# Optimization experiments

Measured on AMD Instinct MI355X. Metric: run time of the kernel, lower is better.

The kernel has to match this reference:

```python
import jax, jax.numpy as jnp
import numpy as np

BIG = 1e30  # stand-in for +inf at DP boundaries (never selected by min)


def setup_inputs() -> dict:
    key = jax.random.key(0)
    kx, kp = jax.random.split(key)
    B, D, T = 32, 16, 1024        # batch, channels (d_patts), stream length
    P, L = 64, 32                 # n_patts, l_patts
    x = jax.random.normal(kx, (B, D, T), dtype=jnp.float32)
    patts = jax.random.normal(kp, (P, D, L), dtype=jnp.float32)
    rho = 0.5
    w = float(rho ** (1.0 / L))   # self.w = rho ** (1 / l_patts)
    return {"x": x, "patts": patts, "w": w}


def _dtw(x, patts, w):
    # Weighted streaming DTW: for each pattern p and each ending time j,
    # D[i, j] = cost[i, j] + min(D[i-1, j], w*D[i, j-1], w*D[i-1, j-1])
    # with D[i, 0] = cost[i, 0] + D[i-1, 0] (first time column cumsum) and
    # cost[i, j] = ||x[:, j] - patts[:, i]||^2 (squared euclidean over channels).
    B, D, T = x.shape
    P, _, L = patts.shape
    p2 = jnp.sum(patts * patts, axis=1)                       # (P, L)

    def cost_at(xj):                                          # xj: (B, D)
        x2 = jnp.sum(xj * xj, axis=1)                         # (B,)
        xp = jnp.einsum('bd,pdl->bpl', xj, patts)             # (B, P, L)
        return x2[:, None, None] + p2[None] - 2.0 * xp        # (B, P, L)

    # first time column
    col0 = jnp.cumsum(cost_at(x[:, :, 0]), axis=-1)           # (B, P, L)

    def step(prev, xj):
        cost = cost_at(xj)                                    # (B, P, L)
        prev_up = jnp.concatenate(
            [jnp.full_like(prev[..., :1], BIG), prev[..., :-1]], axis=-1)
        m = w * jnp.minimum(prev, prev_up)                    # (B, P, L)

        def inner(new_im1, cm):                               # scan along pattern axis
            c_i, m_i = cm
            new_i = c_i + jnp.minimum(new_im1, m_i)
            return new_i, new_i

        _, new = jax.lax.scan(
            inner, jnp.full((B, P), BIG, cost.dtype),
            (jnp.moveaxis(cost, -1, 0), jnp.moveaxis(m, -1, 0)))
        new_col = jnp.moveaxis(new, 0, -1)                    # (B, P, L)
        return new_col, new_col[..., -1]                      # emit full-pattern match cost

    xs = jnp.moveaxis(x[:, :, 1:], -1, 0)                     # (T-1, B, D)
    _, rest = jax.lax.scan(step, col0, xs)                    # (T-1, B, P)
    dtw = jnp.concatenate([col0[None, ..., -1], rest], axis=0)  # (T, B, P)
    return jnp.moveaxis(dtw, 0, -1)                           # (B, P, T)


def reference(x, patts, w):
    return jnp.sqrt(_dtw(x, patts, w))
```

## Files before the change

kernel.cpp:

```cpp
#include <hip/hip_runtime.h>
#include <math.h>

#define B_ 32
#define D_ 16
#define T_ 1024
#define P_ 64
#define L_ 32
#define KB 524288.0f

typedef short short8 __attribute__((ext_vector_type(8)));
typedef float f32x4 __attribute__((ext_vector_type(4)));
typedef unsigned short ushort_t;

template<int CTRL, int ROW_MASK, bool BC>
__device__ __forceinline__ float dpp_mov(float old_, float src) {
  int o = __builtin_bit_cast(int, old_);
  int s = __builtin_bit_cast(int, src);
  int r = __builtin_amdgcn_update_dpp(o, s, CTRL, ROW_MASK, 0xf, BC);
  return __builtin_bit_cast(float, r);
}

__device__ __forceinline__ float scan_sum32(float v) {
  v += dpp_mov<0x111, 0xf, true>(0.f, v);
  v += dpp_mov<0x112, 0xf, true>(0.f, v);
  v += dpp_mov<0x114, 0xf, true>(0.f, v);
  v += dpp_mov<0x118, 0xf, true>(0.f, v);
  v += dpp_mov<0x142, 0xa, false>(0.f, v);
  return v;
}

__device__ __forceinline__ float scan_max32(float v) {
  asm("s_nop 1\n\t"
      "v_max_f32_dpp %0, %0, %0 row_shr:1 row_mask:0xf bank_mask:0xf\n\t"
      "s_nop 1\n\t"
      "v_max_f32_dpp %0, %0, %0 row_shr:2 row_mask:0xf bank_mask:0xf\n\t"
      "s_nop 1\n\t"
      "v_max_f32_dpp %0, %0, %0 row_shr:4 row_mask:0xf bank_mask:0xf\n\t"
      "s_nop 1\n\t"
      "v_max_f32_dpp %0, %0, %0 row_shr:8 row_mask:0xf bank_mask:0xf\n\t"
      "s_nop 1\n\t"
      "v_max_f32_dpp %0, %0, %0 row_bcast:15 row_mask:0xa bank_mask:0xf"
      : "+v"(v));
  return v;
}

__device__ __forceinline__ ushort_t f2bf(float f) {
  unsigned u = __builtin_bit_cast(unsigned, f);
  return (ushort_t)((u + 0x7FFFu + ((u >> 16) & 1u)) >> 16);
}
__device__ __forceinline__ float bf2f(ushort_t h) {
  unsigned u = ((unsigned)h) << 16;
  return __builtin_bit_cast(float, u);
}

__global__ void prep_x(const float* __restrict__ x, ushort_t* __restrict__ xA) {
  int gid = blockIdx.x * blockDim.x + threadIdx.x;
  if (gid >= B_ * T_) return;
  int b = gid >> 10, t = gid & 1023;
  float x2 = 0.f;
  ushort_t o[32];
#pragma unroll
  for (int d = 0; d < 16; ++d) {
    float v = x[((b * 16 + d) << 10) + t];
    x2 = fmaf(v, v, x2);
    o[d] = f2bf(v);
  }
  o[16] = 0x3F80; o[17] = 0x3F80;
  ushort_t hi = f2bf(x2);
  o[18] = hi;
  o[19] = f2bf(x2 - bf2f(hi));
#pragma unroll
  for (int d = 20; d < 32; ++d) o[d] = 0;
  uint4* dst = (uint4*)(xA + (size_t)gid * 32);
#pragma unroll
  for (int q = 0; q < 4; ++q) {
    const ushort_t* s = o + q * 8;
    uint4 u;
    u.x = (unsigned)s[0] | ((unsigned)s[1] << 16);
    u.y = (unsigned)s[2] | ((unsigned)s[3] << 16);
    u.z = (unsigned)s[4] | ((unsigned)s[5] << 16);
    u.w = (unsigned)s[6] | ((unsigned)s[7] << 16);
    dst[q] = u;
  }
}

__global__ __launch_bounds__(64) void prep_patt(const float* __restrict__ patts,
                                                ushort_t* __restrict__ pB) {
  __shared__ float Ls[16 * 33];
  __shared__ float Lh[64];
  __shared__ float LP2[32];

  const int p = blockIdx.x;
  const int l = threadIdx.x;
  const int half = l >> 5;
  const int m = l & 31;

  float p2acc = 0.f;
#pragma unroll
  for (int dd = 0; dd < 16; dd += 2) {
    int d = dd + half;
    float v = patts[((p * 16 + d) << 5) + m];
    p2acc = fmaf(v, v, p2acc);
    Ls[d * 33 + m] = scan_sum32(v);
  }
  Lh[l] = p2acc;
  __syncthreads();
  {
    float tot = Lh[m] + Lh[32 + m];
    float pref = scan_sum32(tot);
    if (half == 0) LP2[m] = pref;
  }
  __syncthreads();

  const int n = l & 15, q = l >> 4;
#pragma unroll
  for (int iblk = 0; iblk < 2; ++iblk) {
    const int i = iblk * 16 + n;
    ushort_t o[8];
    if (q < 2) {
#pragma unroll
      for (int e = 0; e < 8; ++e)
        o[e] = f2bf(-2.f * Ls[(q * 8 + e) * 33 + i]);
    } else if (q == 2) {
      float P2 = LP2[i];
      ushort_t hi = f2bf(P2);
      o[0] = hi; o[1] = f2bf(P2 - bf2f(hi));
      o[2] = f2bf((float)(i + 1)); o[3] = o[2];
      o[4] = o[5] = o[6] = o[7] = 0;
    } else {
#pragma unroll
      for (int e = 0; e < 8; ++e) o[e] = 0;
    }
    uint4 u;
    u.x = (unsigned)o[0] | ((unsigned)o[1] << 16);
    u.y = (unsigned)o[2] | ((unsigned)o[3] << 16);
    u.z = (unsigned)o[4] | ((unsigned)o[5] << 16);
    u.w = (unsigned)o[6] | ((unsigned)o[7] << 16);
    ((uint4*)pB)[(p * 2 + iblk) * 64 + l] = u;
  }
}

__global__ __launch_bounds__(256, 3) void dtw_kernel(
    const ushort_t* __restrict__ xA,
    const ushort_t* __restrict__ pBg,
    const float* __restrict__ wp,
    float* __restrict__ out)
{
  __shared__ float lds[4 * 2640];

  const int tid = threadIdx.x;
  const int l   = tid & 63;
  const int wid = tid >> 6;
  const int li  = l & 31;
  const int g   = l >> 5;
  const int q4  = l >> 4;
  const unsigned bx = blockIdx.x;
  const int ch   = bx % 3u;
  const int rest = bx / 3u;
  const int b     = rest >> 3;
  const int pbase = (rest & 7) << 3;
  const int pA  = pbase + (wid << 1);
  const float w = wp[0];
  const float nw = -w;
  const bool l0c = (li == 0), l31 = (li == 31);

  const int t0    = ch << 4;
  const int warmT = ch ? 16 : 0;

  const short8* pBs = (const short8*)pBg;
  short8 B00 = pBs[((pA    ) * 2 + 0) * 64 + l];
  short8 B01 = pBs[((pA    ) * 2 + 1) * 64 + l];
  short8 B10 = pBs[((pA + 1) * 2 + 0) * 64 + l];
  short8 B11 = pBs[((pA + 1) * 2 + 1) * 64 + l];

  const short8* xAs = (const short8*)xA + ((size_t)b << 12);

  short8 Aa;
  auto loadA = [&](int t) {
    Aa = xAs[((((t0 + t) << 4) + (l & 15)) << 2) + q4];
  };

  float* ldsW = lds + wid * 2640 + 20 + (l & 15) * 20 + q4 * 4;
  const float* ldsR  = lds + wid * 2640 + 20 + g * 660 + li * 20;
  const float* ldsRx = ldsR - 20;

  {
    float* pb = lds + wid * 2640;
    if (l < 20) {
      pb[l] = 0.f; pb[660 + l] = 0.f; pb[1320 + l] = 0.f; pb[1980 + l] = 0.f;
    }
  }
  __syncthreads();

  auto fill = [&](int bufsel) {
    f32x4 z = {0.f, 0.f, 0.f, 0.f};
    float* wb = ldsW + bufsel * 1320;
    f32x4 d0 = __builtin_amdgcn_mfma_f32_16x16x32_bf16(Aa, B00, z, 0, 0, 0);
    f32x4 d1 = __builtin_amdgcn_mfma_f32_16x16x32_bf16(Aa, B01, z, 0, 0, 0);
    f32x4 d2 = __builtin_amdgcn_mfma_f32_16x16x32_bf16(Aa, B10, z, 0, 0, 0);
    f32x4 d3 = __builtin_amdgcn_mfma_f32_16x16x32_bf16(Aa, B11, z, 0, 0, 0);
    *(f32x4*)(wb + 0)   = d0;
    *(f32x4*)(wb + 320) = d1;
    *(f32x4*)(wb + 660) = d2;
    *(f32x4*)(wb + 980) = d3;
  };

  float* orow = out + (((size_t)(b * P_ + pA + g)) << 10) + (t0 << 4);
  float dcur = 0.f;

  auto DP = [&](int bufsel, bool first, bool store, float* op) {
    const float* rb = ldsR  + bufsel * 1320;
    const float* rx = ldsRx + bufsel * 1320;
    f32x4 s0 = *(const f32x4*)(rb + 0);
    f32x4 x0 = *(const f32x4*)(rx + 0);
    f32x4 s1 = *(const f32x4*)(rb + 4);
    f32x4 x1 = *(const f32x4*)(rx + 4);
    f32x4 s2 = *(const f32x4*)(rb + 8);
    f32x4 x2 = *(const f32x4*)(rx + 8);
    f32x4 s3 = *(const f32x4*)(rb + 12);
    f32x4 x3 = *(const f32x4*)(rx + 12);
    float4 r0, r1, r2, r3;
#pragma unroll
    for (int k4 = 0; k4 < 4; ++k4) {
      f32x4 Sq = (k4 == 0) ? s0 : (k4 == 1) ? s1 : (k4 == 2) ? s2 : s3;
      f32x4 Xq = (k4 == 0) ? x0 : (k4 == 1) ? x1 : (k4 == 2) ? x2 : x3;
      float4 rv;
#pragma unroll
      for (int e = 0; e < 4; ++e) {
        float t1  = KB + Xq[e];
        float spk = KB + Sq[e];
        float pu = dpp_mov<0x138, 0xf, true>(0.f, dcur);
        pu = l0c ? dcur : pu;
        float mn = fminf(dcur, pu);
        float u  = fmaf(nw, mn, t1);
        float Mx = scan_max32(u);
        float val = spk - Mx;
        if (first && k4 == 0 && e == 0)
          val = Sq[0];
        dcur = val;
        if (e == 0) rv.x = val; else if (e == 1) rv.y = val;
        else if (e == 2) rv.z = val; else rv.w = val;
      }
      if (k4 == 0) r0 = rv; else if (k4 == 1) r1 = rv;
      else if (k4 == 2) r2 = rv; else r3 = rv;
    }
    if (store) {
      if (l31) {
        float4 s;
        s.x = __builtin_amdgcn_sqrtf(r0.x); s.y = __builtin_amdgcn_sqrtf(r0.y);
        s.z = __builtin_amdgcn_sqrtf(r0.z); s.w = __builtin_amdgcn_sqrtf(r0.w);
        *(float4*)(op + 0) = s;
        s.x = __builtin_amdgcn_sqrtf(r1.x); s.y = __builtin_amdgcn_sqrtf(r1.y);
        s.z = __builtin_amdgcn_sqrtf(r1.z); s.w = __builtin_amdgcn_sqrtf(r1.w);
        *(float4*)(op + 4) = s;
        s.x = __builtin_amdgcn_sqrtf(r2.x); s.y = __builtin_amdgcn_sqrtf(r2.y);
        s.z = __builtin_amdgcn_sqrtf(r2.z); s.w = __builtin_amdgcn_sqrtf(r2.w);
        *(float4*)(op + 8) = s;
        s.x = __builtin_amdgcn_sqrtf(r3.x); s.y = __builtin_amdgcn_sqrtf(r3.y);
        s.z = __builtin_amdgcn_sqrtf(r3.z); s.w = __builtin_amdgcn_sqrtf(r3.w);
        *(float4*)(op + 12) = s;
      }
    }
  };

  loadA(0);
  fill(0);
  loadA(1);
  for (int t = 0; t < 32; ++t) {
    if (t + 1 < 32) fill((t & 1) ^ 1);
    if (t + 2 < 32) loadA(t + 2);
    DP(t & 1, t == 0, t >= warmT, orow + (t << 4));
  }
}

extern "C" void kernel_launch(void* const* d_in, const int* in_sizes, int n_in,
                              void* d_out, int out_size, void* d_ws, size_t ws_size,
                              hipStream_t stream) {
  const float* x     = (const float*)d_in[0];
  const float* patts = (const float*)d_in[1];
  const float* w     = (const float*)d_in[2];
  float* out = (float*)d_out;

  ushort_t* xA = (ushort_t*)d_ws;
  ushort_t* pB = (ushort_t*)((char*)d_ws + (size_t)B_ * T_ * 32 * 2);

  prep_x<<<(B_ * T_ + 255) / 256, 256, 0, stream>>>(x, xA);
  prep_patt<<<P_, 64, 0, stream>>>(patts, pB);
  dtw_kernel<<<B_ * (P_ / 8) * 3, 256, 0, stream>>>(xA, pB, w, out);
}
```

Before: 113.4 us.

## Fuse prep kernels, use single-wave DTW blocks with four uneven time chunks

The two preprocessing kernels become one launch: blocks below 128 pack x and the rest pack four patterns each. The DTW kernel moves from 256-thread blocks covering four pattern pairs to 64-thread single-wave blocks. Time is now split into four overlapping chunks with uneven starts and lengths instead of three equal ones, which gives more and smaller blocks for better CU fill and less per-block latency. The DP inner step is also reformulated: the KB offset is folded into the MFMA accumulator, and the w-scaled min becomes a single max-DPP wave shift, removing a DPP move and a min per step. The extra warmup chunk adds redundant recomputation.

Result: slower. 124.3 us (+9.6%).

```diff
diff --git a/kernel.cpp b/kernel.cpp
--- a/kernel.cpp
+++ b/kernel.cpp
@@ -53,119 +53,118 @@
   return __builtin_bit_cast(float, u);
 }
 
-__global__ void prep_x(const float* __restrict__ x, ushort_t* __restrict__ xA) {
-  int gid = blockIdx.x * blockDim.x + threadIdx.x;
-  if (gid >= B_ * T_) return;
-  int b = gid >> 10, t = gid & 1023;
-  float x2 = 0.f;
-  ushort_t o[32];
-#pragma unroll
-  for (int d = 0; d < 16; ++d) {
-    float v = x[((b * 16 + d) << 10) + t];
-    x2 = fmaf(v, v, x2);
-    o[d] = f2bf(v);
+__global__ __launch_bounds__(256) void prep_fused(
+    const float* __restrict__ x, const float* __restrict__ patts,
+    ushort_t* __restrict__ xA, ushort_t* __restrict__ pB) {
+  const int bid = blockIdx.x;
+  if (bid < 128) {
+    int gid = bid * 256 + threadIdx.x;
+    int b = gid >> 10, t = gid & 1023;
+    float x2 = 0.f;
+    ushort_t o[32];
+#pragma unroll
+    for (int d = 0; d < 16; ++d) {
+      float v = x[((b * 16 + d) << 10) + t];
+      x2 = fmaf(v, v, x2);
+      o[d] = f2bf(v);
+    }
+    o[16] = 0x3F80; o[17] = 0x3F80;
+    ushort_t hi = f2bf(x2);
+    o[18] = hi;
+    o[19] = f2bf(x2 - bf2f(hi));
+#pragma unroll
+    for (int d = 20; d < 32; ++d) o[d] = 0;
+    uint4* dst = (uint4*)(xA + (size_t)gid * 32);
+#pragma unroll
+    for (int q = 0; q < 4; ++q) {
+      const ushort_t* s = o + q * 8;
+      uint4 u;
+      u.x = (unsigned)s[0] | ((unsigned)s[1] << 16);
+      u.y = (unsigned)s[2] | ((unsigned)s[3] << 16);
+      u.z = (unsigned)s[4] | ((unsigned)s[5] << 16);
+      u.w = (unsigned)s[6] | ((unsigned)s[7] << 16);
+      dst[q] = u;
+    }
+  } else {
+    __shared__ float Ls[4][16 * 33];
+    __shared__ float Lh[4][64];
+    __shared__ float LP2[4][32];
+    const int sub = threadIdx.x >> 6;
+    const int l = threadIdx.x & 63;
+    const int p = (bid - 128) * 4 + sub;
+    const int half = l >> 5;
+    const int m = l & 31;
+
+    float p2acc = 0.f;
+#pragma unroll
+    for (int dd = 0; dd < 16; dd += 2) {
+      int d = dd + half;
+      float v = patts[((p * 16 + d) << 5) + m];
+      p2acc = fmaf(v, v, p2acc);
+      Ls[sub][d * 33 + m] = scan_sum32(v);
+    }
+    Lh[sub][l] = p2acc;
+    __syncthreads();
+    {
+      float tot = Lh[sub][m] + Lh[sub][32 + m];
+      float pref = scan_sum32(tot);
+      if (half == 0) LP2[sub][m] = pref;
+    }
+    __syncthreads();
+
+    const int n = l & 15, q = l >> 4;
+#pragma unroll
+    for (int iblk = 0; iblk < 2; ++iblk) {
+      const int i = iblk * 16 + n;
+      ushort_t o[8];
+      if (q < 2) {
+#pragma unroll
+        for (int e = 0; e < 8; ++e)
+          o[e] = f2bf(-2.f * Ls[sub][(q * 8 + e) * 33 + i]);
+      } else if (q == 2) {
+        float P2 = LP2[sub][i];
+        ushort_t hi = f2bf(P2);
+        o[0] = hi; o[1] = f2bf(P2 - bf2f(hi));
+        o[2] = f2bf((float)(i + 1)); o[3] = o[2];
+        o[4] = o[5] = o[6] = o[7] = 0;
+      } else {
+#pragma unroll
+        for (int e = 0; e < 8; ++e) o[e] = 0;
+      }
+      uint4 u;
+      u.x = (unsigned)o[0] | ((unsigned)o[1] << 16);
+      u.y = (unsigned)o[2] | ((unsigned)o[3] << 16);
+      u.z = (unsigned)o[4] | ((unsigned)o[5] << 16);
+      u.w = (unsigned)o[6] | ((unsigned)o[7] << 16);
+      ((uint4*)pB)[(p * 2 + iblk) * 64 + l] = u;
+    }
   }
-  o[16] = 0x3F80; o[17] = 0x3F80;
-  ushort_t hi = f2bf(x2);
-  o[18] = hi;
-  o[19] = f2bf(x2 - bf2f(hi));
-#pragma unroll
-  for (int d = 20; d < 32; ++d) o[d] = 0;
-  uint4* dst = (uint4*)(xA + (size_t)gid * 32);
-#pragma unroll
-  for (int q = 0; q < 4; ++q) {
-    const ushort_t* s = o + q * 8;
-    uint4 u;
-    u.x = (unsigned)s[0] | ((unsigned)s[1] << 16);
-    u.y = (unsigned)s[2] | ((unsigned)s[3] << 16);
-    u.z = (unsigned)s[4] | ((unsigned)s[5] << 16);
-    u.w = (unsigned)s[6] | ((unsigned)s[7] << 16);
-    dst[q] = u;
-  }
-}
-
-__global__ __launch_bounds__(64) void prep_patt(const float* __restrict__ patts,
-                                                ushort_t* __restrict__ pB) {
-  __shared__ float Ls[16 * 33];
-  __shared__ float Lh[64];
-  __shared__ float LP2[32];
-
-  const int p = blockIdx.x;
-  const int l = threadIdx.x;
-  const int half = l >> 5;
-  const int m = l & 31;
-
-  float p2acc = 0.f;
-#pragma unroll
-  for (int dd = 0; dd < 16; dd += 2) {
-    int d = dd + half;
-    float v = patts[((p * 16 + d) << 5) + m];
-    p2acc = fmaf(v, v, p2acc);
-    Ls[d * 33 + m] = scan_sum32(v);
-  }
-  Lh[l] = p2acc;
-  __syncthreads();
-  {
-    float tot = Lh[m] + Lh[32 + m];
-    float pref = scan_sum32(tot);
-    if (half == 0) LP2[m] = pref;
-  }
-  __syncthreads();
-
-  const int n = l & 15, q = l >> 4;
-#pragma unroll
-  for (int iblk = 0; iblk < 2; ++iblk) {
-    const int i = iblk * 16 + n;
-    ushort_t o[8];
-    if (q < 2) {
-#pragma unroll
-      for (int e = 0; e < 8; ++e)
-        o[e] = f2bf(-2.f * Ls[(q * 8 + e) * 33 + i]);
-    } else if (q == 2) {
-      float P2 = LP2[i];
-      ushort_t hi = f2bf(P2);
-      o[0] = hi; o[1] = f2bf(P2 - bf2f(hi));
-      o[2] = f2bf((float)(i + 1)); o[3] = o[2];
-      o[4] = o[5] = o[6] = o[7] = 0;
-    } else {
-#pragma unroll
-      for (int e = 0; e < 8; ++e) o[e] = 0;
-    }
-    uint4 u;
-    u.x = (unsigned)o[0] | ((unsigned)o[1] << 16);
-    u.y = (unsigned)o[2] | ((unsigned)o[3] << 16);
-    u.z = (unsigned)o[4] | ((unsigned)o[5] << 16);
-    u.w = (unsigned)o[6] | ((unsigned)o[7] << 16);
-    ((uint4*)pB)[(p * 2 + iblk) * 64 + l] = u;
-  }
-}
-
-__global__ __launch_bounds__(256, 3) void dtw_kernel(
+}
+
+__global__ __launch_bounds__(64, 4) void dtw_kernel(
     const ushort_t* __restrict__ xA,
     const ushort_t* __restrict__ pBg,
     const float* __restrict__ wp,
     float* __restrict__ out)
 {
-  __shared__ float lds[4 * 2640];
-
-  const int tid = threadIdx.x;
-  const int l   = tid & 63;
-  const int wid = tid >> 6;
+  __shared__ float lds[2640];
+
+  const int l   = threadIdx.x;
   const int li  = l & 31;
   const int g   = l >> 5;
   const int q4  = l >> 4;
   const unsigned bx = blockIdx.x;
-  const int ch   = bx % 3u;
-  const int rest = bx / 3u;
-  const int b     = rest >> 3;
-  const int pbase = (rest & 7) << 3;
-  const int pA  = pbase + (wid << 1);
+  const int ch   = bx & 3u;
+  const unsigned rest = bx >> 2;
+  const int b  = rest >> 5;
+  const int pA = (rest & 31) << 1;
   const float w = wp[0];
   const float nw = -w;
   const bool l0c = (li == 0), l31 = (li == 31);
 
-  const int t0    = ch << 4;
-  const int warmT = ch ? 16 : 0;
+  const int S0    = (ch == 0) ? 0 : (ch == 1) ? 6 : (ch == 2) ? 20 : 34;
+  const int nT    = (ch == 0) ? 22 : 30;
+  const int warmT = (ch == 0) ? 0 : 16;
 
   const short8* pBs = (const short8*)pBg;
   short8 B00 = pBs[((pA    ) * 2 + 0) * 64 + l];
@@ -177,35 +176,33 @@
 
   short8 Aa;
   auto loadA = [&](int t) {
-    Aa = xAs[((((t0 + t) << 4) + (l & 15)) << 2) + q4];
+    Aa = xAs[((((S0 + t) << 4) + (l & 15)) << 2) + q4];
   };
 
-  float* ldsW = lds + wid * 2640 + 20 + (l & 15) * 20 + q4 * 4;
-  const float* ldsR  = lds + wid * 2640 + 20 + g * 660 + li * 20;
+  float* ldsW = lds + 20 + (l & 15) * 20 + q4 * 4;
+  const float* ldsR  = lds + 20 + g * 660 + li * 20;
   const float* ldsRx = ldsR - 20;
 
-  {
-    float* pb = lds + wid * 2640;
-    if (l < 20) {
-      pb[l] = 0.f; pb[660 + l] = 0.f; pb[1320 + l] = 0.f; pb[1980 + l] = 0.f;
-    }
+  if (l < 20) {
+    lds[l] = KB; lds[660 + l] = KB; lds[1320 + l] = KB; lds[1980 + l] = KB;
   }
   __syncthreads();
 
+  const f32x4 zk = {KB, KB, KB, KB};
+
   auto fill = [&](int bufsel) {
-    f32x4 z = {0.f, 0.f, 0.f, 0.f};
     float* wb = ldsW + bufsel * 1320;
-    f32x4 d0 = __builtin_amdgcn_mfma_f32_16x16x32_bf16(Aa, B00, z, 0, 0, 0);
-    f32x4 d1 = __builtin_amdgcn_mfma_f32_16x16x32_bf16(Aa, B01, z, 0, 0, 0);
-    f32x4 d2 = __builtin_amdgcn_mfma_f32_16x16x32_bf16(Aa, B10, z, 0, 0, 0);
-    f32x4 d3 = __builtin_amdgcn_mfma_f32_16x16x32_bf16(Aa, B11, z, 0, 0, 0);
+    f32x4 d0 = __builtin_amdgcn_mfma_f32_16x16x32_bf16(Aa, B00, zk, 0, 0, 0);
+    f32x4 d1 = __builtin_amdgcn_mfma_f32_16x16x32_bf16(Aa, B01, zk, 0, 0, 0);
+    f32x4 d2 = __builtin_amdgcn_mfma_f32_16x16x32_bf16(Aa, B10, zk, 0, 0, 0);
+    f32x4 d3 = __builtin_amdgcn_mfma_f32_16x16x32_bf16(Aa, B11, zk, 0, 0, 0);
     *(f32x4*)(wb + 0)   = d0;
     *(f32x4*)(wb + 320) = d1;
     *(f32x4*)(wb + 660) = d2;
     *(f32x4*)(wb + 980) = d3;
   };
 
-  float* orow = out + (((size_t)(b * P_ + pA + g)) << 10) + (t0 << 4);
+  float* orow = out + (((size_t)(b * P_ + pA + g)) << 10) + (S0 << 4);
   float dcur = 0.f;
 
   auto DP = [&](int bufsel, bool first, bool store, float* op) {
@@ -227,16 +224,19 @@
       float4 rv;
 #pragma unroll
       for (int e = 0; e < 4; ++e) {
-        float t1  = KB + Xq[e];
-        float spk = KB + Sq[e];
-        float pu = dpp_mov<0x138, 0xf, true>(0.f, dcur);
-        pu = l0c ? dcur : pu;
-        float mn = fminf(dcur, pu);
-        float u  = fmaf(nw, mn, t1);
+        float Zo = Sq[e];
+        float Zx = Xq[e];
+        float a = fmaf(nw, dcur, Zx);
+        float c = fmaf(nw, dcur, Zo);
+        float u;
+        asm("s_nop 1\n\t"
+            "v_max_f32_dpp %0, %1, %2 wave_shr:1 row_mask:0xf bank_mask:0xf"
+            : "=&v"(u) : "v"(c), "v"(a));
+        u = l0c ? a : u;
         float Mx = scan_max32(u);
-        float val = spk - Mx;
+        float val = Zo - Mx;
         if (first && k4 == 0 && e == 0)
-          val = Sq[0];
+          val = Zo - KB;
         dcur = val;
         if (e == 0) rv.x = val; else if (e == 1) rv.y = val;
         else if (e == 2) rv.z = val; else rv.w = val;
@@ -266,9 +266,9 @@
   loadA(0);
   fill(0);
   loadA(1);
-  for (int t = 0; t < 32; ++t) {
-    if (t + 1 < 32) fill((t & 1) ^ 1);
-    if (t + 2 < 32) loadA(t + 2);
+  for (int t = 0; t < nT; ++t) {
+    if (t + 1 < nT) fill((t & 1) ^ 1);
+    if (t + 2 < nT) loadA(t + 2);
     DP(t & 1, t == 0, t >= warmT, orow + (t << 4));
   }
 }
@@ -284,7 +284,6 @@
   ushort_t* xA = (ushort_t*)d_ws;
   ushort_t* pB = (ushort_t*)((char*)d_ws + (size_t)B_ * T_ * 32 * 2);
 
-  prep_x<<<(B_ * T_ + 255) / 256, 256, 0, stream>>>(x, xA);
-  prep_patt<<<P_, 64, 0, stream>>>(patts, pB);
-  dtw_kernel<<<B_ * (P_ / 8) * 3, 256, 0, stream>>>(xA, pB, w, out);
-}
+  prep_fused<<<144, 256, 0, stream>>>(x, patts, xA, pB);
+  dtw_kernel<<<B_ * (P_ / 2) * 4, 64, 0, stream>>>(xA, pB, w, out);
+}
```
